# Performance work log

Measured on AMD Instinct MI355X. Metric: run time of the kernel, lower is better.

The kernel has to match this reference:

```python
import jax, jax.numpy as jnp
import numpy as np

B, S, D, H = 2, 4096, 256, 4
DH = D // H  # head dim = 64


def setup_inputs() -> dict:
    key = jax.random.key(0)
    ks = jax.random.split(key, 7)
    scale = 1.0 / np.sqrt(D)
    return {
        "x": jax.random.normal(ks[0], (B, S, D), dtype=jnp.float32),
        "Wq": jax.random.normal(ks[1], (D, D), dtype=jnp.float32) * scale,
        "bq": jax.random.normal(ks[2], (D,), dtype=jnp.float32) * scale,
        "Wk": jax.random.normal(ks[3], (D, D), dtype=jnp.float32) * scale,
        "bk": jax.random.normal(ks[4], (D,), dtype=jnp.float32) * scale,
        "Wv": jax.random.normal(ks[5], (D, D), dtype=jnp.float32) * scale,
        "bv": jax.random.normal(ks[6], (D,), dtype=jnp.float32) * scale,
    }


def reference(x, Wq, bq, Wk, bk, Wv, bv):
    b, s, d = x.shape
    # torch Linear: y = x @ W.T + b ; W stored as [out, in]
    q = (jnp.einsum('bsd,ed->bse', x, Wq) + bq).reshape(b, s, H, DH)
    k = (jnp.einsum('bsd,ed->bse', x, Wk) + bk).reshape(b, s, H, DH)
    v = (jnp.einsum('bsd,ed->bse', x, Wv) + bv).reshape(b, s, H, DH)
    # scores: [b, s(query), t(key), h]
    scores = jnp.einsum('bshd,bthd->bsth', q, k) / jnp.sqrt(jnp.float32(DH))
    # softmax over key axis t (dim=-2 in torch layout bsth)
    weights = jax.nn.softmax(scores, axis=2)
    out = jnp.einsum('bsth,bthd->bshd', weights, v)
    return out.reshape(b, s, d)
```

## Files before the change

### kernel.cpp

```cpp
#include <hip/hip_runtime.h>

#define S_LEN 4096
#define D_MODEL 256
#define NH 4
#define DH 64
#define CSC 0.18033688011112042f

typedef __attribute__((ext_vector_type(8))) short bf16x8;
typedef __attribute__((ext_vector_type(8))) unsigned short u16x8;
typedef __attribute__((ext_vector_type(4))) float f32x4;
typedef __attribute__((ext_vector_type(16))) float f32x16;
typedef __attribute__((ext_vector_type(2))) unsigned int u32x2;
typedef __attribute__((ext_vector_type(4))) unsigned int u32x4;

#define MFMA16(a, b, c) __builtin_amdgcn_mfma_f32_16x16x32_bf16((a), (b), (c), 0, 0, 0)
#define MFMA32(a, b, c) __builtin_amdgcn_mfma_f32_32x32x16_bf16((a), (b), (c), 0, 0, 0)
#define SWZ(r, c) ((c) ^ (((r) & 7) << 3))

static __device__ __forceinline__ unsigned short f2bf(float f) {
  unsigned int u = __float_as_uint(f);
  u += 0x7fffu + ((u >> 16) & 1u);
  return (unsigned short)(u >> 16);
}

static __device__ __forceinline__ unsigned int pack2(float lo, float hi) {
  return ((unsigned int)f2bf(hi) << 16) | (unsigned int)f2bf(lo);
}

static __device__ __forceinline__ unsigned int cvtpk(float lo, float hi) {
  unsigned int r;
  asm("v_cvt_pk_bf16_f32 %0, %1, %2" : "=v"(r) : "v"(lo), "v"(hi));
  return r;
}

static __device__ __forceinline__ u16x8 cvt8(float4 a, float4 b) {
  u16x8 v;
  v[0] = f2bf(a.x); v[1] = f2bf(a.y); v[2] = f2bf(a.z); v[3] = f2bf(a.w);
  v[4] = f2bf(b.x); v[5] = f2bf(b.y); v[6] = f2bf(b.z); v[7] = f2bf(b.w);
  return v;
}

__global__ __launch_bounds__(256) void prep(
    const float* __restrict__ Wq, const float* __restrict__ Wk,
    const float* __restrict__ Wv, unsigned short* __restrict__ Wb)
{
  const int gid = blockIdx.x * 256 + threadIdx.x;
  const int l   = gid & 63;
  const int f   = gid >> 6;
  const int kk  = f & 7;
  const int ctn = f >> 3;
  const int ct  = ctn & 3, nt = ctn >> 2;
  const int pj  = nt >> 2, h = nt & 3;
  const float* Wsel = (pj == 0) ? Wq : (pj == 1) ? Wk : Wv;
  const float* src =
      Wsel + (size_t)(h * 64 + ct * 16 + (l & 15)) * D_MODEL + kk * 32 + (l >> 4) * 8;
  float4 a = *(const float4*)src;
  float4 b = *(const float4*)(src + 4);
  *(u16x8*)(Wb + (size_t)gid * 8) = cvt8(a, b);
}

__global__ __launch_bounds__(256) void qkv_proj(
    const float* __restrict__ x, const unsigned short* __restrict__ Wb,
    const float* __restrict__ bq, const float* __restrict__ bk,
    const float* __restrict__ bv,
    unsigned short* __restrict__ Qh, unsigned short* __restrict__ Kh,
    unsigned short* __restrict__ Vt)
{
  __shared__ unsigned short xs[32][264];

  const int tid  = threadIdx.x;
  const int lane = tid & 63;
  const int w    = tid >> 6;
  const int r16  = lane & 15;
  const int hi   = lane >> 4;
  const int m0   = (blockIdx.x >> 1) * 32;
  const int ntB  = (blockIdx.x & 1) * 6;

  {
    const int r  = tid >> 3;
    const int c0 = (tid & 7) * 32;
    const float* xp = x + (size_t)(m0 + r) * D_MODEL + c0;
#pragma unroll
    for (int i = 0; i < 32; i += 8) {
      float4 a = *(const float4*)(xp + i);
      float4 b = *(const float4*)(xp + i + 4);
      *(u16x8*)&xs[r][c0 + i] = cvt8(a, b);
    }
  }
  __syncthreads();

  const int bb = m0 >> 12;
  const int s_base = m0 & 4095;

#pragma unroll
  for (int t = 0; t < 6; ++t) {
    const int nt = ntB + t, pj = nt >> 2, h = nt & 3;
    f32x4 acc[2] = {};
    const size_t fb = (size_t)(nt * 4 + w) * 8;
#pragma unroll
    for (int kk = 0; kk < 8; ++kk) {
      bf16x8 bw = *(const bf16x8*)(Wb + (fb + kk) * 512 + lane * 8);
#pragma unroll
      for (int rt = 0; rt < 2; ++rt) {
        bf16x8 af = *(const bf16x8*)&xs[rt * 16 + r16][kk * 32 + hi * 8];
        acc[rt] = MFMA16(af, bw, acc[rt]);
      }
    }
    const float* bsel = (pj == 0) ? bq : (pj == 1) ? bk : bv;
    const float bias = bsel[h * 64 + w * 16 + r16];

    if (pj < 2) {
      unsigned short* dst = (pj == 0) ? Qh : Kh;
      const float sc = (pj == 0) ? CSC : 1.0f;
#pragma unroll
      for (int rt = 0; rt < 2; ++rt)
#pragma unroll
        for (int j = 0; j < 4; ++j) {
          int s = s_base + rt * 16 + hi * 4 + j;
          dst[((size_t)(bb * NH + h) * S_LEN + s) * DH + w * 16 + r16] =
              f2bf((acc[rt][j] + bias) * sc);
        }
    } else {
      unsigned short* dst = Vt + ((size_t)(bb * NH + h) * DH + w * 16 + r16) * S_LEN;
#pragma unroll
      for (int rt = 0; rt < 2; ++rt) {
        int s0 = s_base + rt * 16 + hi * 4;
        uint2 uu;
        uu.x = pack2(acc[rt][0] + bias, acc[rt][1] + bias);
        uu.y = pack2(acc[rt][2] + bias, acc[rt][3] + bias);
        *(uint2*)(dst + s0) = uu;
      }
    }
  }
}

__global__ __launch_bounds__(1024) void attn(
    const unsigned short* __restrict__ Qh,
    const unsigned short* __restrict__ Kh,
    const unsigned short* __restrict__ Vt,
    float* __restrict__ out)
{
  __shared__ unsigned short KVs[2][2][4][64][64];

  const int tid = threadIdx.x;
  const int ln  = tid & 63;
  const int wv  = tid >> 6;
  const int g   = wv >> 2;
  const int wq  = wv & 3;
  const int r32 = ln & 31;
  const int h   = ln >> 5;

  const int bid = blockIdx.x;
  const int bh  = bid & 7;
  const int q0  = (bid >> 3) * 128;

  const unsigned short* Qb = Qh + (size_t)bh * S_LEN * DH;
  const unsigned short* Kb = Kh + (size_t)bh * S_LEN * DH;
  const unsigned short* Vb = Vt + (size_t)bh * DH * S_LEN;

  const int q = q0 + wq * 32 + r32;
  bf16x8 qf[4];
#pragma unroll
  for (int s = 0; s < 4; ++s)
    qf[s] = *(const bf16x8*)(Qb + (size_t)q * DH + s * 16 + h * 8);

  f32x16 o0 = {}, o1 = {};
  float l_run = 0.f;

  const int u  = tid & 255;
  const int sr = u >> 2;
  const int sc = (u & 3) * 16;

  uint4 kA, kB, vA, vB;
  {
    const unsigned short* kp = Kb + ((size_t)(g * 64 + sr)) * DH + sc;
    kA = *(const uint4*)kp;  kB = *(const uint4*)(kp + 8);
    const unsigned short* vp = Vb + (size_t)sr * S_LEN + g * 64 + sc;
    vA = *(const uint4*)vp;  vB = *(const uint4*)(vp + 8);
  }
  *(uint4*)&KVs[0][0][g][sr][SWZ(sr, sc)]     = kA;
  *(uint4*)&KVs[0][0][g][sr][SWZ(sr, sc + 8)] = kB;
  *(uint4*)&KVs[1][0][g][sr][SWZ(sr, sc)]     = vA;
  *(uint4*)&KVs[1][0][g][sr][SWZ(sr, sc + 8)] = vB;
  {
    const int c = 4 + g;
    const unsigned short* kp = Kb + ((size_t)(c * 64 + sr)) * DH + sc;
    kA = *(const uint4*)kp;  kB = *(const uint4*)(kp + 8);
    const unsigned short* vp = Vb + (size_t)sr * S_LEN + c * 64 + sc;
    vA = *(const uint4*)vp;  vB = *(const uint4*)(vp + 8);
  }

  for (int it = 0; it < 16; ++it) {
    __syncthreads();
    if (it < 15) {
      const int nb = (it + 1) & 1;
      *(uint4*)&KVs[0][nb][g][sr][SWZ(sr, sc)]     = kA;
      *(uint4*)&KVs[0][nb][g][sr][SWZ(sr, sc + 8)] = kB;
      *(uint4*)&KVs[1][nb][g][sr][SWZ(sr, sc)]     = vA;
      *(uint4*)&KVs[1][nb][g][sr][SWZ(sr, sc + 8)] = vB;
      int c = 4 * (it + 2) + g;  if (c > 63) c = 63;
      const unsigned short* kp = Kb + ((size_t)(c * 64 + sr)) * DH + sc;
      kA = *(const uint4*)kp;  kB = *(const uint4*)(kp + 8);
      const unsigned short* vp = Vb + (size_t)sr * S_LEN + c * 64 + sc;
      vA = *(const uint4*)vp;  vB = *(const uint4*)(vp + 8);
    }
    const int tb = it & 1;

    f32x16 s0 = {}, s1 = {};
    __builtin_amdgcn_s_setprio(1);
#pragma unroll
    for (int s = 0; s < 4; ++s) {
      bf16x8 a0 = *(const bf16x8*)&KVs[0][tb][g][r32][SWZ(r32, s * 16 + h * 8)];
      bf16x8 a1 = *(const bf16x8*)&KVs[0][tb][g][32 + r32][SWZ(r32, s * 16 + h * 8)];
      s0 = MFMA32(a0, qf[s], s0);
      s1 = MFMA32(a1, qf[s], s1);
    }
    __builtin_amdgcn_s_setprio(0);

    float ps = 0.f;
#pragma unroll
    for (int i = 0; i < 16; ++i) {
      s0[i] = __builtin_amdgcn_exp2f(s0[i]);  ps += s0[i];
      s1[i] = __builtin_amdgcn_exp2f(s1[i]);  ps += s1[i];
    }
    l_run += ps;

    unsigned int u0[8], u1[8];
#pragma unroll
    for (int gg = 0; gg < 4; ++gg) {
      u0[gg * 2 + 0] = cvtpk(s0[4 * gg + 0], s0[4 * gg + 1]);
      u0[gg * 2 + 1] = cvtpk(s0[4 * gg + 2], s0[4 * gg + 3]);
      u1[gg * 2 + 0] = cvtpk(s1[4 * gg + 0], s1[4 * gg + 1]);
      u1[gg * 2 + 1] = cvtpk(s1[4 * gg + 2], s1[4 * gg + 3]);
    }
    bf16x8 pb[4];
#pragma unroll
    for (int S = 0; S < 2; ++S) {
      u32x2 w0 = __builtin_amdgcn_permlane32_swap(u0[4 * S + 0], u0[4 * S + 2], false, false);
      u32x2 w1 = __builtin_amdgcn_permlane32_swap(u0[4 * S + 1], u0[4 * S + 3], false, false);
      u32x4 t0; t0[0] = w0[0]; t0[1] = w1[0]; t0[2] = w0[1]; t0[3] = w1[1];
      pb[S] = __builtin_bit_cast(bf16x8, t0);
      u32x2 w2 = __builtin_amdgcn_permlane32_swap(u1[4 * S + 0], u1[4 * S + 2], false, false);
      u32x2 w3 = __builtin_amdgcn_permlane32_swap(u1[4 * S + 1], u1[4 * S + 3], false, false);
      u32x4 t1; t1[0] = w2[0]; t1[1] = w3[0]; t1[2] = w2[1]; t1[3] = w3[1];
      pb[2 + S] = __builtin_bit_cast(bf16x8, t1);
    }

    __builtin_amdgcn_s_setprio(1);
#pragma unroll
    for (int s = 0; s < 4; ++s) {
      bf16x8 a0 = *(const bf16x8*)&KVs[1][tb][g][r32][SWZ(r32, s * 16 + h * 8)];
      bf16x8 a1 = *(const bf16x8*)&KVs[1][tb][g][32 + r32][SWZ(r32, s * 16 + h * 8)];
      o0 = MFMA32(a0, pb[s], o0);
      o1 = MFMA32(a1, pb[s], o1);
    }
    __builtin_amdgcn_s_setprio(0);
  }

  __syncthreads();
  float* cb = (float*)&KVs[0][0][0][0][0];
  const int cbase = wq * 64 + ln;

  if (g >= 2) {
    const int base = ((g - 2) * 256 + cbase) * 33;
#pragma unroll
    for (int i = 0; i < 16; ++i) { cb[base + i] = o0[i]; cb[base + 16 + i] = o1[i]; }
    cb[base + 32] = l_run;
  }
  __syncthreads();
  if (g < 2) {
    const int base = (g * 256 + cbase) * 33;
#pragma unroll
    for (int i = 0; i < 16; ++i) { o0[i] += cb[base + i]; o1[i] += cb[base + 16 + i]; }
    l_run += cb[base + 32];
  }
  __syncthreads();
  if (g == 1) {
    const int base = cbase * 33;
#pragma unroll
    for (int i = 0; i < 16; ++i) { cb[base + i] = o0[i]; cb[base + 16 + i] = o1[i]; }
    cb[base + 32] = l_run;
  }
  __syncthreads();
  if (g == 0) {
    const int base = cbase * 33;
#pragma unroll
    for (int i = 0; i < 16; ++i) { o0[i] += cb[base + i]; o1[i] += cb[base + 16 + i]; }
    l_run += cb[base + 32];

    const float lt  = l_run + __shfl_xor(l_run, 32);
    const float inv = 1.f / lt;
    const int bb = bh >> 2, hd = bh & 3;
    float* op = out + ((size_t)(bb * S_LEN + q)) * D_MODEL + hd * DH;
#pragma unroll
    for (int gg = 0; gg < 4; ++gg) {
      float4 v0, v1;
      v0.x = o0[4 * gg + 0] * inv;  v0.y = o0[4 * gg + 1] * inv;
      v0.z = o0[4 * gg + 2] * inv;  v0.w = o0[4 * gg + 3] * inv;
      *(float4*)(op + 8 * gg + 4 * h) = v0;
      v1.x = o1[4 * gg + 0] * inv;  v1.y = o1[4 * gg + 1] * inv;
      v1.z = o1[4 * gg + 2] * inv;  v1.w = o1[4 * gg + 3] * inv;
      *(float4*)(op + 32 + 8 * gg + 4 * h) = v1;
    }
  }
}

extern "C" void kernel_launch(void* const* d_in, const int* in_sizes, int n_in,
                              void* d_out, int out_size, void* d_ws, size_t ws_size,
                              hipStream_t stream) {
  const float* x  = (const float*)d_in[0];
  const float* Wq = (const float*)d_in[1];
  const float* bq = (const float*)d_in[2];
  const float* Wk = (const float*)d_in[3];
  const float* bk = (const float*)d_in[4];
  const float* Wv = (const float*)d_in[5];
  const float* bv = (const float*)d_in[6];
  float* out = (float*)d_out;

  const size_t per = (size_t)2 * NH * S_LEN * DH;
  if (ws_size < 3 * per * sizeof(unsigned short)) return;
  unsigned short* Qh = (unsigned short*)d_ws;
  unsigned short* Kh = Qh + per;
  unsigned short* Vt = Kh + per;
  unsigned short* Wb = (unsigned short*)d_out;

  prep<<<96, 256, 0, stream>>>(Wq, Wk, Wv, Wb);
  qkv_proj<<<512, 256, 0, stream>>>(x, Wb, bq, bk, bv, Qh, Kh, Vt);
  attn<<<256, 1024, 0, stream>>>(Qh, Kh, Vt, out);
}
```

Measured before the change: 65.41 us.

## Store K/V tiles in MFMA fragment order and stage QKV outputs via LDS

Result: slower. 100.1 us (+53.1%).

```diff
diff --git a/kernel.cpp b/kernel.cpp
--- a/kernel.cpp
+++ b/kernel.cpp
@@ -5,6 +5,7 @@
 #define NH 4
 #define DH 64
 #define CSC 0.18033688011112042f
+#define FRAG 520
 
 typedef __attribute__((ext_vector_type(8))) short bf16x8;
 typedef __attribute__((ext_vector_type(8))) unsigned short u16x8;
@@ -15,16 +16,11 @@
 
 #define MFMA16(a, b, c) __builtin_amdgcn_mfma_f32_16x16x32_bf16((a), (b), (c), 0, 0, 0)
 #define MFMA32(a, b, c) __builtin_amdgcn_mfma_f32_32x32x16_bf16((a), (b), (c), 0, 0, 0)
-#define SWZ(r, c) ((c) ^ (((r) & 7) << 3))
 
 static __device__ __forceinline__ unsigned short f2bf(float f) {
   unsigned int u = __float_as_uint(f);
   u += 0x7fffu + ((u >> 16) & 1u);
   return (unsigned short)(u >> 16);
-}
-
-static __device__ __forceinline__ unsigned int pack2(float lo, float hi) {
-  return ((unsigned int)f2bf(hi) << 16) | (unsigned int)f2bf(lo);
 }
 
 static __device__ __forceinline__ unsigned int cvtpk(float lo, float hi) {
@@ -38,6 +34,29 @@
   v[0] = f2bf(a.x); v[1] = f2bf(a.y); v[2] = f2bf(a.z); v[3] = f2bf(a.w);
   v[4] = f2bf(b.x); v[5] = f2bf(b.y); v[6] = f2bf(b.z); v[7] = f2bf(b.w);
   return v;
+}
+
+static __device__ __forceinline__ void pack_pb(const f32x16& s0, const f32x16& s1,
+                                               bf16x8* pb) {
+  unsigned int u0[8], u1[8];
+#pragma unroll
+  for (int gg = 0; gg < 4; ++gg) {
+    u0[gg * 2 + 0] = cvtpk(s0[4 * gg + 0], s0[4 * gg + 1]);
+    u0[gg * 2 + 1] = cvtpk(s0[4 * gg + 2], s0[4 * gg + 3]);
+    u1[gg * 2 + 0] = cvtpk(s1[4 * gg + 0], s1[4 * gg + 1]);
+    u1[gg * 2 + 1] = cvtpk(s1[4 * gg + 2], s1[4 * gg + 3]);
+  }
+#pragma unroll
+  for (int S = 0; S < 2; ++S) {
+    u32x2 w0 = __builtin_amdgcn_permlane32_swap(u0[4 * S + 0], u0[4 * S + 2], false, false);
+    u32x2 w1 = __builtin_amdgcn_permlane32_swap(u0[4 * S + 1], u0[4 * S + 3], false, false);
+    u32x4 t0; t0[0] = w0[0]; t0[1] = w1[0]; t0[2] = w0[1]; t0[3] = w1[1];
+    pb[S] = __builtin_bit_cast(bf16x8, t0);
+    u32x2 w2 = __builtin_amdgcn_permlane32_swap(u1[4 * S + 0], u1[4 * S + 2], false, false);
+    u32x2 w3 = __builtin_amdgcn_permlane32_swap(u1[4 * S + 1], u1[4 * S + 3], false, false);
+    u32x4 t1; t1[0] = w2[0]; t1[1] = w3[0]; t1[2] = w2[1]; t1[3] = w3[1];
+    pb[2 + S] = __builtin_bit_cast(bf16x8, t1);
+  }
 }
 
 __global__ __launch_bounds__(256) void prep(
@@ -67,6 +86,7 @@
     unsigned short* __restrict__ Vt)
 {
   __shared__ unsigned short xs[32][264];
+  __shared__ float tbuf[32][68];
 
   const int tid  = threadIdx.x;
   const int lane = tid & 63;
@@ -92,7 +112,6 @@
   const int bb = m0 >> 12;
   const int s_base = m0 & 4095;
 
-#pragma unroll
   for (int t = 0; t < 6; ++t) {
     const int nt = ntB + t, pj = nt >> 2, h = nt & 3;
     f32x4 acc[2] = {};
@@ -108,29 +127,32 @@
     }
     const float* bsel = (pj == 0) ? bq : (pj == 1) ? bk : bv;
     const float bias = bsel[h * 64 + w * 16 + r16];
+    const float scl  = (pj == 0) ? CSC : 1.0f;
+
+#pragma unroll
+    for (int rt = 0; rt < 2; ++rt)
+#pragma unroll
+      for (int j = 0; j < 4; ++j)
+        tbuf[rt * 16 + hi * 4 + j][w * 16 + r16] = (acc[rt][j] + bias) * scl;
+    __syncthreads();
 
     if (pj < 2) {
-      unsigned short* dst = (pj == 0) ? Qh : Kh;
-      const float sc = (pj == 0) ? CSC : 1.0f;
-#pragma unroll
-      for (int rt = 0; rt < 2; ++rt)
-#pragma unroll
-        for (int j = 0; j < 4; ++j) {
-          int s = s_base + rt * 16 + hi * 4 + j;
-          dst[((size_t)(bb * NH + h) * S_LEN + s) * DH + w * 16 + r16] =
-              f2bf((acc[rt][j] + bias) * sc);
-        }
+      const int s_l = tid >> 3, c0 = (tid & 7) * 8;
+      float4 a = *(const float4*)&tbuf[s_l][c0];
+      float4 b = *(const float4*)&tbuf[s_l][c0 + 4];
+      unsigned short* dst = ((pj == 0) ? Qh : Kh) +
+          ((size_t)(bb * NH + h) * S_LEN + s_base + s_l) * DH + c0;
+      *(u16x8*)dst = cvt8(a, b);
     } else {
-      unsigned short* dst = Vt + ((size_t)(bb * NH + h) * DH + w * 16 + r16) * S_LEN;
-#pragma unroll
-      for (int rt = 0; rt < 2; ++rt) {
-        int s0 = s_base + rt * 16 + hi * 4;
-        uint2 uu;
-        uu.x = pack2(acc[rt][0] + bias, acc[rt][1] + bias);
-        uu.y = pack2(acc[rt][2] + bias, acc[rt][3] + bias);
-        *(uint2*)(dst + s0) = uu;
-      }
-    }
+      const int d_l = tid & 63, sblk = (tid >> 6) * 8;
+      u16x8 vv;
+#pragma unroll
+      for (int e = 0; e < 8; ++e) vv[e] = f2bf(tbuf[sblk + e][d_l]);
+      unsigned short* dst = Vt +
+          ((size_t)(bb * NH + h) * DH + d_l) * S_LEN + s_base + sblk;
+      *(u16x8*)dst = vv;
+    }
+    __syncthreads();
   }
 }
 
@@ -140,7 +162,7 @@
     const unsigned short* __restrict__ Vt,
     float* __restrict__ out)
 {
-  __shared__ unsigned short KVs[2][2][4][64][64];
+  __shared__ unsigned short KV[2][2][4][8 * FRAG];
 
   const int tid = threadIdx.x;
   const int ln  = tid & 63;
@@ -168,50 +190,52 @@
   float l_run = 0.f;
 
   const int u  = tid & 255;
+  const int gs = tid >> 8;
   const int sr = u >> 2;
   const int sc = (u & 3) * 16;
-
-  uint4 kA, kB, vA, vB;
-  {
-    const unsigned short* kp = Kb + ((size_t)(g * 64 + sr)) * DH + sc;
-    kA = *(const uint4*)kp;  kB = *(const uint4*)(kp + 8);
-    const unsigned short* vp = Vb + (size_t)sr * S_LEN + g * 64 + sc;
-    vA = *(const uint4*)vp;  vB = *(const uint4*)(vp + 8);
-  }
-  *(uint4*)&KVs[0][0][g][sr][SWZ(sr, sc)]     = kA;
-  *(uint4*)&KVs[0][0][g][sr][SWZ(sr, sc + 8)] = kB;
-  *(uint4*)&KVs[1][0][g][sr][SWZ(sr, sc)]     = vA;
-  *(uint4*)&KVs[1][0][g][sr][SWZ(sr, sc + 8)] = vB;
-  {
-    const int c = 4 + g;
-    const unsigned short* kp = Kb + ((size_t)(c * 64 + sr)) * DH + sc;
-    kA = *(const uint4*)kp;  kB = *(const uint4*)(kp + 8);
-    const unsigned short* vp = Vb + (size_t)sr * S_LEN + c * 64 + sc;
-    vA = *(const uint4*)vp;  vB = *(const uint4*)(vp + 8);
-  }
+  int off[2];
+#pragma unroll
+  for (int m = 0; m < 2; ++m) {
+    const int d0 = sc + 8 * m;
+    const int f  = (d0 >> 4) * 2 + (sr >> 5);
+    const int la = (sr & 31) + 32 * ((d0 >> 3) & 1);
+    off[m] = f * FRAG + la * 8;
+  }
+
+  uint4 kst[2], vst[2];
+#define LOAD_CHUNK(c)                                                            \
+  { const unsigned short* kp = Kb + ((size_t)(c) * 64 + sr) * DH + sc;           \
+    kst[0] = *(const uint4*)kp;  kst[1] = *(const uint4*)(kp + 8);               \
+    const unsigned short* vp = Vb + (size_t)sr * S_LEN + (c) * 64 + sc;          \
+    vst[0] = *(const uint4*)vp;  vst[1] = *(const uint4*)(vp + 8); }
+#define STAGE(par)                                                               \
+  { _Pragma("unroll")                                                            \
+    for (int m = 0; m < 2; ++m) {                                                \
+      *(uint4*)&KV[par][0][gs][off[m]] = kst[m];                                 \
+      *(uint4*)&KV[par][1][gs][off[m]] = vst[m];                                 \
+    } }
+
+  LOAD_CHUNK(gs);
+  STAGE(0);
+  LOAD_CHUNK(4 + gs);
 
   for (int it = 0; it < 16; ++it) {
     __syncthreads();
     if (it < 15) {
-      const int nb = (it + 1) & 1;
-      *(uint4*)&KVs[0][nb][g][sr][SWZ(sr, sc)]     = kA;
-      *(uint4*)&KVs[0][nb][g][sr][SWZ(sr, sc + 8)] = kB;
-      *(uint4*)&KVs[1][nb][g][sr][SWZ(sr, sc)]     = vA;
-      *(uint4*)&KVs[1][nb][g][sr][SWZ(sr, sc + 8)] = vB;
-      int c = 4 * (it + 2) + g;  if (c > 63) c = 63;
-      const unsigned short* kp = Kb + ((size_t)(c * 64 + sr)) * DH + sc;
-      kA = *(const uint4*)kp;  kB = *(const uint4*)(kp + 8);
-      const unsigned short* vp = Vb + (size_t)sr * S_LEN + c * 64 + sc;
-      vA = *(const uint4*)vp;  vB = *(const uint4*)(vp + 8);
-    }
-    const int tb = it & 1;
+      STAGE((it + 1) & 1);
+      int c = 4 * (it + 2) + gs;  if (c > 63) c = 63;
+      LOAD_CHUNK(c);
+    }
+    const unsigned short* Kc = &KV[it & 1][0][g][0];
+    const unsigned short* Vc = &KV[it & 1][1][g][0];
+    const int lb = ln * 8;
 
     f32x16 s0 = {}, s1 = {};
     __builtin_amdgcn_s_setprio(1);
 #pragma unroll
     for (int s = 0; s < 4; ++s) {
-      bf16x8 a0 = *(const bf16x8*)&KVs[0][tb][g][r32][SWZ(r32, s * 16 + h * 8)];
-      bf16x8 a1 = *(const bf16x8*)&KVs[0][tb][g][32 + r32][SWZ(r32, s * 16 + h * 8)];
+      bf16x8 a0 = *(const bf16x8*)(Kc + lb + (2 * s + 0) * FRAG);
+      bf16x8 a1 = *(const bf16x8*)(Kc + lb + (2 * s + 1) * FRAG);
       s0 = MFMA32(a0, qf[s], s0);
       s1 = MFMA32(a1, qf[s], s1);
     }
@@ -225,40 +249,22 @@
     }
     l_run += ps;
 
-    unsigned int u0[8], u1[8];
-#pragma unroll
-    for (int gg = 0; gg < 4; ++gg) {
-      u0[gg * 2 + 0] = cvtpk(s0[4 * gg + 0], s0[4 * gg + 1]);
-      u0[gg * 2 + 1] = cvtpk(s0[4 * gg + 2], s0[4 * gg + 3]);
-      u1[gg * 2 + 0] = cvtpk(s1[4 * gg + 0], s1[4 * gg + 1]);
-      u1[gg * 2 + 1] = cvtpk(s1[4 * gg + 2], s1[4 * gg + 3]);
-    }
     bf16x8 pb[4];
-#pragma unroll
-    for (int S = 0; S < 2; ++S) {
-      u32x2 w0 = __builtin_amdgcn_permlane32_swap(u0[4 * S + 0], u0[4 * S + 2], false, false);
-      u32x2 w1 = __builtin_amdgcn_permlane32_swap(u0[4 * S + 1], u0[4 * S + 3], false, false);
-      u32x4 t0; t0[0] = w0[0]; t0[1] = w1[0]; t0[2] = w0[1]; t0[3] = w1[1];
-      pb[S] = __builtin_bit_cast(bf16x8, t0);
-      u32x2 w2 = __builtin_amdgcn_permlane32_swap(u1[4 * S + 0], u1[4 * S + 2], false, false);
-      u32x2 w3 = __builtin_amdgcn_permlane32_swap(u1[4 * S + 1], u1[4 * S + 3], false, false);
-      u32x4 t1; t1[0] = w2[0]; t1[1] = w3[0]; t1[2] = w2[1]; t1[3] = w3[1];
-      pb[2 + S] = __builtin_bit_cast(bf16x8, t1);
-    }
+    pack_pb(s0, s1, pb);
 
     __builtin_amdgcn_s_setprio(1);
 #pragma unroll
     for (int s = 0; s < 4; ++s) {
-      bf16x8 a0 = *(const bf16x8*)&KVs[1][tb][g][r32][SWZ(r32, s * 16 + h * 8)];
-      bf16x8 a1 = *(const bf16x8*)&KVs[1][tb][g][32 + r32][SWZ(r32, s * 16 + h * 8)];
-      o0 = MFMA32(a0, pb[s], o0);
-      o1 = MFMA32(a1, pb[s], o1);
+      bf16x8 b0 = *(const bf16x8*)(Vc + lb + (2 * s + 0) * FRAG);
+      bf16x8 b1 = *(const bf16x8*)(Vc + lb + (2 * s + 1) * FRAG);
+      o0 = MFMA32(b0, pb[s], o0);
+      o1 = MFMA32(b1, pb[s], o1);
     }
     __builtin_amdgcn_s_setprio(0);
   }
 
   __syncthreads();
-  float* cb = (float*)&KVs[0][0][0][0][0];
+  float* cb = (float*)&KV[0][0][0][0];
   const int cbase = wq * 64 + ln;
 
   if (g >= 2) {
```
